# Optimization experiments

Measured on AMD Instinct MI355X. Metric: run time of the kernel, lower is better.

Reference implementation:

```python
import jax, jax.numpy as jnp
import numpy as np

EPS = 1e-7
MAX_TANH = 15.0
C = 1.0  # curvature of every PoincareBall manifold in the stack

def _norm(x):
    return jnp.clip(jnp.linalg.norm(x, axis=-1, keepdims=True), EPS, None)

def _artanh(x):
    return jnp.arctanh(jnp.clip(x, -1.0 + 1e-5, 1.0 - 1e-5))

def proj(x, c=C):
    # clip points back inside the Poincare ball
    maxnorm = (1.0 - 1e-5) / jnp.sqrt(c)
    n = _norm(x)
    return jnp.where(n > maxnorm, x / n * maxnorm, x)

def expmap0(u, c=C):
    sc = jnp.sqrt(c)
    n = _norm(u)
    return jnp.tanh(jnp.clip(sc * n, -MAX_TANH, MAX_TANH)) * u / (sc * n)

def logmap0(x, c=C):
    sc = jnp.sqrt(c)
    n = _norm(x)
    return _artanh(sc * n) * x / (sc * n)

def mobius_add(x, y, c=C):
    x2 = jnp.sum(x * x, -1, keepdims=True)
    y2 = jnp.sum(y * y, -1, keepdims=True)
    xy = jnp.sum(x * y, -1, keepdims=True)
    num = (1 + 2 * c * xy + c * y2) * x + (1 - c * x2) * y
    den = 1 + 2 * c * xy + c * c * x2 * y2
    return num / jnp.clip(den, EPS, None)

def mobius_matvec(W, x, c=C):
    sc = jnp.sqrt(c)
    xn = _norm(x)
    mx = x @ W.T
    mxn = _norm(mx)
    return jnp.tanh(jnp.clip(mxn / xn * _artanh(sc * xn), -MAX_TANH, MAX_TANH)) * mx / (mxn * sc)

def hgc_layer(x, edges, node_mask, edge_mask, W, b, c_in=C, c_out=C):
    n_nodes = x.shape[0]
    # HypLinear: mobius matvec + hyperbolic bias add
    h = proj(mobius_matvec(W, x, c_in), c_in)
    hyp_bias = proj(expmap0(b[None, :], c_in), c_in)
    h = proj(mobius_add(h, hyp_bias, c_in), c_in)
    # HypAgg: masked tangent-space mean over incoming edges (gather -> segment_sum)
    row, col = edges[0], edges[1]
    ht = logmap0(h, c_in)                 # [N, d] tangent features
    msgs = ht[col] * edge_mask            # [E, d]
    agg = jax.ops.segment_sum(msgs, row, num_segments=n_nodes)
    deg = jax.ops.segment_sum(edge_mask, row, num_segments=n_nodes)
    agg = agg / jnp.clip(deg, 1.0, None)
    h = proj(expmap0(agg, c_in), c_in)
    # HypAct: nonlinearity in tangent space, re-map to output manifold
    xt = jax.nn.relu(logmap0(h, c_in))
    h = proj(expmap0(xt, c_out), c_out)
    return h * node_mask

N_NODES = 50000
N_EDGES = 1200000
DIM = 64
NUM_LAYERS = 2

def setup_inputs() -> dict:
    key = jax.random.key(0)
    ks = jax.random.split(key, 8)
    h_tan = 0.1 * jax.random.normal(ks[0], (N_NODES, DIM), dtype=jnp.float32)
    h = proj(expmap0(h_tan))  # valid Poincare-ball points
    distances = jax.random.uniform(ks[1], (N_EDGES, 1), dtype=jnp.float32)
    edges = jax.random.randint(ks[2], (2, N_EDGES), 0, N_NODES, dtype=jnp.int64)
    node_mask = jnp.ones((N_NODES, 1), dtype=jnp.float32)
    edge_mask = jnp.ones((N_EDGES, 1), dtype=jnp.float32)
    W0 = 0.1 * jax.random.normal(ks[3], (DIM, DIM), dtype=jnp.float32)
    b0 = 0.01 * jax.random.normal(ks[4], (DIM,), dtype=jnp.float32)
    W1 = 0.1 * jax.random.normal(ks[5], (DIM, DIM), dtype=jnp.float32)
    b1 = 0.01 * jax.random.normal(ks[6], (DIM,), dtype=jnp.float32)
    return {"h": h, "distances": distances, "edges": edges,
            "node_mask": node_mask, "edge_mask": edge_mask,
            "W0": W0, "b0": b0, "W1": W1, "b1": b1}

def reference(h, distances, edges, node_mask, edge_mask, W0, b0, W1, b1):
    # nn.Sequential of HyperbolicGraphConvolution layers; distances/edges/masks pass through
    out = hgc_layer(h, edges, node_mask, edge_mask, W0, b0)
    out = hgc_layer(out, edges, node_mask, edge_mask, W1, b1)
    return out
```

## Files before the change

kernel.cpp:

```cpp
#include <hip/hip_runtime.h>
#include <hip/hip_fp16.h>

#define EPS      1e-7f
#define MAX_TANH 15.0f
#define MAXNORM  0.99999f
#define ART_CLIP 0.99999f
#define HGRID    512
#define CAPF     8192

__device__ __forceinline__ float wave_sum64(float v) {
#pragma unroll
    for (int o = 32; o > 0; o >>= 1) v += __shfl_xor(v, o, 64);
    return v;
}

__device__ __forceinline__ float gsum16(float v) {
    v += __shfl_xor(v, 1, 64);
    v += __shfl_xor(v, 2, 64);
    v += __shfl_xor(v, 4, 64);
    v += __shfl_xor(v, 8, 64);
    return v;
}

__device__ __forceinline__ float clamp_tanh_arg(float x) {
    return fminf(fmaxf(x, -MAX_TANH), MAX_TANH);
}

__device__ __forceinline__ float artanh_clip(float x) {
    x = fminf(fmaxf(x, -ART_CLIP), ART_CLIP);
    return 0.5f * logf((1.0f + x) / (1.0f - x));
}

__device__ __forceinline__ void fma_h4(float4& acc, uint2 u, float m) {
    float2 f01 = __half22float2(*reinterpret_cast<__half2*>(&u.x));
    float2 f23 = __half22float2(*reinterpret_cast<__half2*>(&u.y));
    acc.x = fmaf(f01.x, m, acc.x); acc.y = fmaf(f01.y, m, acc.y);
    acc.z = fmaf(f23.x, m, acc.z); acc.w = fmaf(f23.y, m, acc.w);
}

__global__ __launch_bounds__(256) void hist_transform_kernel(
    const int* __restrict__ rows, int* __restrict__ histB,
    int n_edges, int epb, int nb,
    const float* __restrict__ x, const float* __restrict__ W,
    const float* __restrict__ b, __half* __restrict__ ht, int n_nodes)
{
    __shared__ float WT[64 * 65];
    __shared__ float xs[4][64];
    __shared__ int hh[256];

    if (blockIdx.x < HGRID) {
        const int b0 = blockIdx.x * epb;
        const int b1 = min(b0 + epb, n_edges);
        if (threadIdx.x < 256) hh[threadIdx.x] = 0;
        __syncthreads();
        for (int i = b0 + threadIdx.x; i < b1; i += 256)
            atomicAdd(&hh[rows[i] >> 8], 1);
        __syncthreads();
        if (threadIdx.x < nb)
            histB[blockIdx.x * nb + threadIdx.x] = hh[threadIdx.x];
        return;
    }

    const int t = threadIdx.x;
    const int lane = t & 63;
    const int wv = t >> 6;
    const int bid = blockIdx.x - HGRID;
    const int tgrid = gridDim.x - HGRID;

#pragma unroll
    for (int r = 0; r < 16; ++r) {
        int idx = r * 256 + t;
        WT[(idx & 63) * 65 + (idx >> 6)] = W[idx];
    }
    __syncthreads();

    float bj = b[lane];
    float bn = fmaxf(sqrtf(wave_sum64(bj * bj)), EPS);
    float tb = tanhf(clamp_tanh_arg(bn));
    float hb = tb * bj / bn;
    if (tb > MAXNORM) { hb *= MAXNORM / tb; tb = MAXNORM; }
    const float y2 = tb * tb;

    for (long long base = (long long)bid * 4; base < n_nodes;
         base += (long long)tgrid * 4) {
        long long node = base + wv;
        float xj = 0.0f;
        if (node < n_nodes) xj = x[node * 64 + lane];
        xs[wv][lane] = xj;

        float mxj = 0.0f;
#pragma unroll
        for (int k = 0; k < 64; ++k)
            mxj = fmaf(xs[wv][k], WT[k * 65 + lane], mxj);

        float xn  = fmaxf(sqrtf(wave_sum64(xj * xj)), EPS);
        float mxn = fmaxf(sqrtf(wave_sum64(mxj * mxj)), EPS);
        float r = tanhf(clamp_tanh_arg(mxn / xn * artanh_clip(xn)));
        float hj = r * mxj / mxn;
        float hn = fmaxf(r, EPS);
        if (hn > MAXNORM) { hj *= MAXNORM / hn; hn = MAXNORM; }

        float x2 = hn * hn;
        float xy = wave_sum64(hj * hb);
        float num = (1.0f + 2.0f * xy + y2) * hj + (1.0f - x2) * hb;
        float den = fmaxf(1.0f + 2.0f * xy + x2 * y2, EPS);
        hj = num / den;

        float hn2 = fmaxf(sqrtf(wave_sum64(hj * hj)), EPS);
        if (hn2 > MAXNORM) { hj *= MAXNORM / hn2; hn2 = MAXNORM; }

        float htj = artanh_clip(hn2) * hj / hn2;

        if (node < n_nodes) ht[node * 64 + lane] = __float2half(htj);
    }
}

__global__ __launch_bounds__(HGRID) void scan_bucket_kernel(
    int* __restrict__ histB, int* __restrict__ tot, int nb)
{
    __shared__ int wsum[8];
    const int b = blockIdx.x;
    const int t = threadIdx.x;
    const int lane = t & 63, wid = t >> 6;
    int v = histB[t * nb + b];
    int incl = v;
#pragma unroll
    for (int o = 1; o < 64; o <<= 1) {
        int tt = __shfl_up(incl, o, 64);
        if (lane >= o) incl += tt;
    }
    if (lane == 63) wsum[wid] = incl;
    __syncthreads();
    if (wid == 0 && lane < 8) {
        int ws = wsum[lane];
#pragma unroll
        for (int o = 1; o < 8; o <<= 1) {
            int tt = __shfl_up(ws, o, 64);
            if (lane >= o) ws += tt;
        }
        wsum[lane] = ws;
    }
    __syncthreads();
    int base = (wid > 0) ? wsum[wid - 1] : 0;
    histB[t * nb + b] = base + incl - v;
    if (t == HGRID - 1) tot[b] = base + incl;
}

__global__ __launch_bounds__(256) void scan_base_kernel(
    const int* __restrict__ tot, int* __restrict__ bucket_base, int nb)
{
    __shared__ int s[256];
    const int t = threadIdx.x;
    int v = (t < nb) ? tot[t] : 0;
    s[t] = v;
    __syncthreads();
    for (int off = 1; off < 256; off <<= 1) {
        int u = (t >= off) ? s[t - off] : 0;
        __syncthreads();
        s[t] += u;
        __syncthreads();
    }
    if (t < nb) bucket_base[t] = s[t] - v;
    if (t == nb - 1) bucket_base[nb] = s[t];
}

__global__ __launch_bounds__(256) void coarse_scatter_kernel(
    const int* __restrict__ rows, const int* __restrict__ cols,
    const float* __restrict__ edge_mask, const int* __restrict__ off,
    const int* __restrict__ bucket_base,
    int2* __restrict__ coarse, int n_edges, int epb, int nb)
{
    __shared__ int cur[256];
    const int b0 = blockIdx.x * epb;
    const int b1 = min(b0 + epb, n_edges);
    if (threadIdx.x < nb)
        cur[threadIdx.x] = bucket_base[threadIdx.x] + off[blockIdx.x * nb + threadIdx.x];
    __syncthreads();
    for (int i = b0 + threadIdx.x; i < b1; i += 256) {
        int r = rows[i], c = cols[i];
        float m = edge_mask[i];
        int pos = atomicAdd(&cur[r >> 8], 1);
        coarse[pos] = make_int2((r << 16) | c, __float_as_int(m));
    }
}

__global__ __launch_bounds__(1024) void fine_kernel(
    const int2* __restrict__ coarse, const int* __restrict__ bucket_base,
    int2* __restrict__ csr, int* __restrict__ row_start, int n_nodes, int n_edges)
{
    __shared__ int hh[256], incl[256], curs[256];
    __shared__ int2 out[CAPF];
    const int t = threadIdx.x;
    const int b = blockIdx.x;
    const int bbase = bucket_base[b];
    const int n_e = bucket_base[b + 1] - bbase;

    if (t < 256) hh[t] = 0;
    __syncthreads();
    for (int i = t; i < n_e; i += 1024) {
        unsigned rx = (unsigned)coarse[bbase + i].x;
        atomicAdd(&hh[(rx >> 16) & 255], 1);
    }
    __syncthreads();
    if (t < 256) incl[t] = hh[t];
    __syncthreads();
    for (int off = 1; off < 256; off <<= 1) {
        int v = 0;
        if (t < 256 && t >= off) v = incl[t - off];
        __syncthreads();
        if (t < 256) incl[t] += v;
        __syncthreads();
    }
    if (t < 256) {
        int lstart = incl[t] - hh[t];
        curs[t] = lstart;
        int grow = (b << 8) + t;
        if (grow < n_nodes) row_start[grow] = bbase + lstart;
    }
    if (b == gridDim.x - 1 && t == 0) row_start[n_nodes] = n_edges;
    __syncthreads();
    for (int i = t; i < n_e; i += 1024) {
        int2 rec = coarse[bbase + i];
        unsigned rx = (unsigned)rec.x;
        int slot = atomicAdd(&curs[(rx >> 16) & 255], 1);
        if (slot < CAPF) out[slot] = make_int2((int)(rx & 0xffffu), rec.y);
    }
    __syncthreads();
    const int lim = min(n_e, CAPF);
    for (int i = t; i < lim; i += 1024)
        csr[bbase + i] = out[i];
}

template <bool FUSE>
__global__ __launch_bounds__(256) void gather_kernel(
    const __half* __restrict__ ht, const int2* __restrict__ csr,
    const int* __restrict__ row_start, const float* __restrict__ node_mask,
    const float* __restrict__ W, const float* __restrict__ b,
    void* __restrict__ outp, int n_nodes)
{
    __shared__ float WT[FUSE ? 4096 : 1];
    __shared__ float xs[FUSE ? 16 * 68 : 1];

    const int t = threadIdx.x;
    const int lane = t & 63;
    const int wv = t >> 6;
    const int ns = lane >> 4;
    const int q  = lane & 15;

    float4 hb4 = make_float4(0.f, 0.f, 0.f, 0.f);
    float y2 = 0.f;
    if constexpr (FUSE) {
#pragma unroll
        for (int r = 0; r < 16; ++r) {
            int idx = r * 256 + t;
            int j = idx >> 6, k = idx & 63;
            WT[(k << 6) | (j ^ ((k & 15) << 2))] = W[idx];
        }
        float4 b4 = ((const float4*)b)[q];
        float ssb = b4.x*b4.x + b4.y*b4.y + b4.z*b4.z + b4.w*b4.w;
        float bn = fmaxf(sqrtf(gsum16(ssb)), EPS);
        float tb = tanhf(clamp_tanh_arg(bn));
        float sb = tb / bn;
        hb4.x = b4.x * sb; hb4.y = b4.y * sb; hb4.z = b4.z * sb; hb4.w = b4.w * sb;
        if (tb > MAXNORM) {
            float sc = MAXNORM / tb;
            hb4.x *= sc; hb4.y *= sc; hb4.z *= sc; hb4.w *= sc;
            tb = MAXNORM;
        }
        y2 = tb * tb;
        __syncthreads();
    }

    const int node = blockIdx.x * 16 + (wv << 2) + ns;
    const bool valid = node < n_nodes;
    const int nd = valid ? node : (n_nodes - 1);
    const int s = row_start[nd];
    const int e = row_start[nd + 1];

    float4 acc = make_float4(0.f, 0.f, 0.f, 0.f);
    float msum = 0.f;
    int j = s;
    for (; j + 4 <= e; j += 4) {
        int2 c0 = csr[j], c1 = csr[j + 1];
        int2 c2 = csr[j + 2], c3 = csr[j + 3];
        uint2 u0 = *((const uint2*)(ht + (long long)c0.x * 64) + q);
        uint2 u1 = *((const uint2*)(ht + (long long)c1.x * 64) + q);
        uint2 u2 = *((const uint2*)(ht + (long long)c2.x * 64) + q);
        uint2 u3 = *((const uint2*)(ht + (long long)c3.x * 64) + q);
        float m0 = __int_as_float(c0.y), m1 = __int_as_float(c1.y);
        float m2 = __int_as_float(c2.y), m3 = __int_as_float(c3.y);
        fma_h4(acc, u0, m0);
        fma_h4(acc, u1, m1);
        fma_h4(acc, u2, m2);
        fma_h4(acc, u3, m3);
        msum += m0 + m1 + m2 + m3;
    }
    for (; j < e; ++j) {
        int2 cm = csr[j];
        uint2 u = *((const uint2*)(ht + (long long)cm.x * 64) + q);
        float m = __int_as_float(cm.y);
        fma_h4(acc, u, m);
        msum += m;
    }

    const float inv = 1.0f / fmaxf(msum, 1.0f);
    acc.x *= inv; acc.y *= inv; acc.z *= inv; acc.w *= inv;

    float ss = acc.x*acc.x + acc.y*acc.y + acc.z*acc.z + acc.w*acc.w;
    float n1 = fmaxf(sqrtf(gsum16(ss)), EPS);
    float t1 = tanhf(clamp_tanh_arg(n1));
    float r1 = t1 / n1;
    acc.x *= r1; acc.y *= r1; acc.z *= r1; acc.w *= r1;
    if (t1 > MAXNORM) {
        float sc = MAXNORM / t1;
        acc.x *= sc; acc.y *= sc; acc.z *= sc; acc.w *= sc;
        t1 = MAXNORM;
    }
    float n2 = fmaxf(t1, EPS);
    float r2 = artanh_clip(n2) / n2;
    acc.x = fmaxf(acc.x * r2, 0.f); acc.y = fmaxf(acc.y * r2, 0.f);
    acc.z = fmaxf(acc.z * r2, 0.f); acc.w = fmaxf(acc.w * r2, 0.f);

    ss = acc.x*acc.x + acc.y*acc.y + acc.z*acc.z + acc.w*acc.w;
    float n3 = fmaxf(sqrtf(gsum16(ss)), EPS);
    float t3 = tanhf(clamp_tanh_arg(n3));
    float r3 = t3 / n3;
    acc.x *= r3; acc.y *= r3; acc.z *= r3; acc.w *= r3;
    if (t3 > MAXNORM) {
        float sc = MAXNORM / t3;
        acc.x *= sc; acc.y *= sc; acc.z *= sc; acc.w *= sc;
        t3 = MAXNORM;
    }

    const float nm = node_mask[nd];
    acc.x *= nm; acc.y *= nm; acc.z *= nm; acc.w *= nm;

    if constexpr (!FUSE) {
        if (valid) ((float4*)((float*)outp + (long long)node * 64))[q] = acc;
    } else {
        float* xrow = &xs[(wv * 4 + ns) * 68];
        *(float4*)(xrow + (q << 2)) = acc;

        float4 mx = make_float4(0.f, 0.f, 0.f, 0.f);
#pragma unroll
        for (int k = 0; k < 64; ++k) {
            float xk = xrow[k];
            const float4 w4 = *(const float4*)&WT[(k << 6) | ((q << 2) ^ ((k & 15) << 2))];
            mx.x = fmaf(w4.x, xk, mx.x); mx.y = fmaf(w4.y, xk, mx.y);
            mx.z = fmaf(w4.z, xk, mx.z); mx.w = fmaf(w4.w, xk, mx.w);
        }

        float xn  = fmaxf(t3 * fabsf(nm), EPS);
        float ssm = mx.x*mx.x + mx.y*mx.y + mx.z*mx.z + mx.w*mx.w;
        float mxn = fmaxf(sqrtf(gsum16(ssm)), EPS);
        float r = tanhf(clamp_tanh_arg(mxn / xn * artanh_clip(xn)));
        float rs = r / mxn;
        float4 hj = make_float4(mx.x * rs, mx.y * rs, mx.z * rs, mx.w * rs);
        float hn = fmaxf(r, EPS);
        if (hn > MAXNORM) {
            float sc = MAXNORM / hn;
            hj.x *= sc; hj.y *= sc; hj.z *= sc; hj.w *= sc;
            hn = MAXNORM;
        }

        float x2 = hn * hn;
        float xy = gsum16(hj.x*hb4.x + hj.y*hb4.y + hj.z*hb4.z + hj.w*hb4.w);
        float ca = 1.0f + 2.0f * xy + y2;
        float cb = 1.0f - x2;
        float iden = 1.0f / fmaxf(1.0f + 2.0f * xy + x2 * y2, EPS);
        hj.x = (ca * hj.x + cb * hb4.x) * iden;
        hj.y = (ca * hj.y + cb * hb4.y) * iden;
        hj.z = (ca * hj.z + cb * hb4.z) * iden;
        hj.w = (ca * hj.w + cb * hb4.w) * iden;

        float ssh = hj.x*hj.x + hj.y*hj.y + hj.z*hj.z + hj.w*hj.w;
        float hn2 = fmaxf(sqrtf(gsum16(ssh)), EPS);
        float sc2 = (hn2 > MAXNORM) ? (MAXNORM / hn2) : 1.0f;
        float hnc = fminf(hn2, MAXNORM);
        float lr = artanh_clip(hnc) / hnc * sc2;
        hj.x *= lr; hj.y *= lr; hj.z *= lr; hj.w *= lr;

        if (valid) {
            __half2 p01 = __float22half2_rn(make_float2(hj.x, hj.y));
            __half2 p23 = __float22half2_rn(make_float2(hj.z, hj.w));
            uint2 o;
            o.x = *reinterpret_cast<unsigned*>(&p01);
            o.y = *reinterpret_cast<unsigned*>(&p23);
            *((uint2*)((__half*)outp + (long long)node * 64) + q) = o;
        }
    }
}

extern "C" void kernel_launch(void* const* d_in, const int* in_sizes, int n_in,
                              void* d_out, int out_size, void* d_ws, size_t ws_size,
                              hipStream_t stream) {
    const float* h         = (const float*)d_in[0];
    const int*   edges     = (const int*)d_in[2];
    const float* node_mask = (const float*)d_in[3];
    const float* edge_mask = (const float*)d_in[4];
    const float* W0        = (const float*)d_in[5];
    const float* b0        = (const float*)d_in[6];
    const float* W1        = (const float*)d_in[7];
    const float* b1        = (const float*)d_in[8];
    float* out = (float*)d_out;

    const int N = in_sizes[0] / 64;
    const int E = in_sizes[4];
    const int* rows = edges;
    const int* cols = edges + E;

    const int NB  = (N + 255) >> 8;
    const int EPB = (E + HGRID - 1) / HGRID;

    size_t nd = (size_t)N * 64;
    char* ws = (char*)d_ws;
    __half* B1         = (__half*)ws; ws += nd * sizeof(__half);
    __half* B2         = (__half*)ws; ws += nd * sizeof(__half);
    int2*  coarse      = (int2*)ws;   ws += (size_t)E * sizeof(int2);
    int2*  csr         = (int2*)ws;   ws += (size_t)E * sizeof(int2);
    int*   histB       = (int*)ws;    ws += (size_t)HGRID * NB * sizeof(int);
    int*   tot         = (int*)ws;    ws += (size_t)NB * sizeof(int);
    int*   bucket_base = (int*)ws;    ws += (size_t)(NB + 1) * sizeof(int);
    int*   row_start   = (int*)ws;    ws += (size_t)(N + 1) * sizeof(int);

    const int TGRID = 1024;
    const int NGRID = (N + 15) / 16;

    hist_transform_kernel<<<HGRID + TGRID, 256, 0, stream>>>(
        rows, histB, E, EPB, NB, h, W0, b0, B1, N);

    scan_bucket_kernel<<<NB, HGRID, 0, stream>>>(histB, tot, NB);

    scan_base_kernel<<<1, 256, 0, stream>>>(tot, bucket_base, NB);

    coarse_scatter_kernel<<<HGRID, 256, 0, stream>>>(
        rows, cols, edge_mask, histB, bucket_base, coarse, E, EPB, NB);

    fine_kernel<<<NB, 1024, 0, stream>>>(
        coarse, bucket_base, csr, row_start, N, E);

    gather_kernel<true><<<NGRID, 256, 0, stream>>>(
        B1, csr, row_start, node_mask, W1, b1, B2, N);

    gather_kernel<false><<<NGRID, 256, 0, stream>>>(
        B2, csr, row_start, node_mask, nullptr, nullptr, out, N);
}
```

Measured before the change: 222.2 us.

## Fuse fine CSR bucketing with first-layer gather and compact CSR to 32-bit

Bucket size drops from 256 to 128 rows, so each fine-sort block keeps its sorted edges in shared memory. The first-layer aggregation and second-layer transform then run inside that same block, reading edges from LDS and skipping a separate CSR read pass. The CSR written for the second layer packs the column and an fp16 edge mask into 32 bits, halving index traffic. In exchange, each block uses a lot of shared memory at 1024 threads, which lowers occupancy. The edge mask is rounded to fp16, and the 16-bit column packing relies on node IDs below 65536.

```diff
diff --git a/kernel.cpp b/kernel.cpp
--- a/kernel.cpp
+++ b/kernel.cpp
@@ -6,7 +6,9 @@
 #define MAXNORM  0.99999f
 #define ART_CLIP 0.99999f
 #define HGRID    512
-#define CAPF     8192
+#define RPB      128
+#define CAPF     4096
+#define NBMAX    512
 
 __device__ __forceinline__ float wave_sum64(float v) {
 #pragma unroll
@@ -46,18 +48,18 @@
 {
     __shared__ float WT[64 * 65];
     __shared__ float xs[4][64];
-    __shared__ int hh[256];
+    __shared__ int hh[NBMAX];
 
     if (blockIdx.x < HGRID) {
         const int b0 = blockIdx.x * epb;
         const int b1 = min(b0 + epb, n_edges);
-        if (threadIdx.x < 256) hh[threadIdx.x] = 0;
+        for (int j = threadIdx.x; j < nb; j += 256) hh[j] = 0;
         __syncthreads();
         for (int i = b0 + threadIdx.x; i < b1; i += 256)
-            atomicAdd(&hh[rows[i] >> 8], 1);
+            atomicAdd(&hh[rows[i] >> 7], 1);
         __syncthreads();
-        if (threadIdx.x < nb)
-            histB[blockIdx.x * nb + threadIdx.x] = hh[threadIdx.x];
+        for (int j = threadIdx.x; j < nb; j += 256)
+            histB[blockIdx.x * nb + j] = hh[j];
         return;
     }
 
@@ -146,15 +148,15 @@
     if (t == HGRID - 1) tot[b] = base + incl;
 }
 
-__global__ __launch_bounds__(256) void scan_base_kernel(
+__global__ __launch_bounds__(NBMAX) void scan_base_kernel(
     const int* __restrict__ tot, int* __restrict__ bucket_base, int nb)
 {
-    __shared__ int s[256];
+    __shared__ int s[NBMAX];
     const int t = threadIdx.x;
     int v = (t < nb) ? tot[t] : 0;
     s[t] = v;
     __syncthreads();
-    for (int off = 1; off < 256; off <<= 1) {
+    for (int off = 1; off < NBMAX; off <<= 1) {
         int u = (t >= off) ? s[t - off] : 0;
         __syncthreads();
         s[t] += u;
@@ -170,175 +172,158 @@
     const int* __restrict__ bucket_base,
     int2* __restrict__ coarse, int n_edges, int epb, int nb)
 {
-    __shared__ int cur[256];
+    __shared__ int cur[NBMAX];
     const int b0 = blockIdx.x * epb;
     const int b1 = min(b0 + epb, n_edges);
-    if (threadIdx.x < nb)
-        cur[threadIdx.x] = bucket_base[threadIdx.x] + off[blockIdx.x * nb + threadIdx.x];
+    for (int j = threadIdx.x; j < nb; j += 256)
+        cur[j] = bucket_base[j] + off[blockIdx.x * nb + j];
     __syncthreads();
     for (int i = b0 + threadIdx.x; i < b1; i += 256) {
         int r = rows[i], c = cols[i];
         float m = edge_mask[i];
-        int pos = atomicAdd(&cur[r >> 8], 1);
+        int pos = atomicAdd(&cur[r >> 7], 1);
         coarse[pos] = make_int2((r << 16) | c, __float_as_int(m));
     }
 }
 
-__global__ __launch_bounds__(1024) void fine_kernel(
+__global__ __launch_bounds__(1024) void fine_gather_kernel(
     const int2* __restrict__ coarse, const int* __restrict__ bucket_base,
-    int2* __restrict__ csr, int* __restrict__ row_start, int n_nodes, int n_edges)
+    const __half* __restrict__ ht1, const float* __restrict__ node_mask,
+    const float* __restrict__ W, const float* __restrict__ bvec,
+    unsigned* __restrict__ csr4, int* __restrict__ row_start,
+    __half* __restrict__ ht2, int n_nodes, int n_edges)
 {
-    __shared__ int hh[256], incl[256], curs[256];
-    __shared__ int2 out[CAPF];
+    __shared__ int hh[RPB], incl[RPB], curs[RPB];
+    __shared__ int2 outE[CAPF];
+    __shared__ float WT[4096];
+    __shared__ float xs[64 * 68];
+
     const int t = threadIdx.x;
     const int b = blockIdx.x;
+    const int q = t & 15;
+    const int g = t >> 4;
     const int bbase = bucket_base[b];
     const int n_e = bucket_base[b + 1] - bbase;
 
-    if (t < 256) hh[t] = 0;
-    __syncthreads();
-    for (int i = t; i < n_e; i += 1024) {
-        unsigned rx = (unsigned)coarse[bbase + i].x;
-        atomicAdd(&hh[(rx >> 16) & 255], 1);
-    }
-    __syncthreads();
-    if (t < 256) incl[t] = hh[t];
-    __syncthreads();
-    for (int off = 1; off < 256; off <<= 1) {
-        int v = 0;
-        if (t < 256 && t >= off) v = incl[t - off];
+#pragma unroll
+    for (int r = 0; r < 4; ++r) {
+        int idx = r * 1024 + t;
+        int j = idx >> 6, k = idx & 63;
+        WT[(k << 6) | (j ^ ((k & 15) << 2))] = W[idx];
+    }
+    float4 b4 = ((const float4*)bvec)[q];
+    float ssb = b4.x*b4.x + b4.y*b4.y + b4.z*b4.z + b4.w*b4.w;
+    float bn = fmaxf(sqrtf(gsum16(ssb)), EPS);
+    float tb = tanhf(clamp_tanh_arg(bn));
+    float sb = tb / bn;
+    float4 hb4 = make_float4(b4.x * sb, b4.y * sb, b4.z * sb, b4.w * sb);
+    if (tb > MAXNORM) {
+        float sc = MAXNORM / tb;
+        hb4.x *= sc; hb4.y *= sc; hb4.z *= sc; hb4.w *= sc;
+        tb = MAXNORM;
+    }
+    const float y2 = tb * tb;
+
+    if (t < RPB) hh[t] = 0;
+    __syncthreads();
+    for (int i = t; i < n_e; i += 1024)
+        atomicAdd(&hh[(coarse[bbase + i].x >> 16) & (RPB - 1)], 1);
+    __syncthreads();
+    if (t < RPB) incl[t] = hh[t];
+    __syncthreads();
+    for (int off = 1; off < RPB; off <<= 1) {
+        int v = (t < RPB && t >= off) ? incl[t - off] : 0;
         __syncthreads();
-        if (t < 256) incl[t] += v;
+        if (t < RPB) incl[t] += v;
         __syncthreads();
     }
-    if (t < 256) {
-        int lstart = incl[t] - hh[t];
-        curs[t] = lstart;
-        int grow = (b << 8) + t;
-        if (grow < n_nodes) row_start[grow] = bbase + lstart;
+    if (t < RPB) {
+        curs[t] = incl[t] - hh[t];
+        int grow = (b << 7) + t;
+        if (grow < n_nodes) row_start[grow] = bbase + incl[t] - hh[t];
     }
     if (b == gridDim.x - 1 && t == 0) row_start[n_nodes] = n_edges;
     __syncthreads();
     for (int i = t; i < n_e; i += 1024) {
         int2 rec = coarse[bbase + i];
-        unsigned rx = (unsigned)rec.x;
-        int slot = atomicAdd(&curs[(rx >> 16) & 255], 1);
-        if (slot < CAPF) out[slot] = make_int2((int)(rx & 0xffffu), rec.y);
-    }
-    __syncthreads();
+        int slot = atomicAdd(&curs[(rec.x >> 16) & (RPB - 1)], 1);
+        if (slot < CAPF) outE[slot] = make_int2(rec.x & 0xffff, rec.y);
+    }
+    __syncthreads();
+
     const int lim = min(n_e, CAPF);
-    for (int i = t; i < lim; i += 1024)
-        csr[bbase + i] = out[i];
-}
-
-template <bool FUSE>
-__global__ __launch_bounds__(256) void gather_kernel(
-    const __half* __restrict__ ht, const int2* __restrict__ csr,
-    const int* __restrict__ row_start, const float* __restrict__ node_mask,
-    const float* __restrict__ W, const float* __restrict__ b,
-    void* __restrict__ outp, int n_nodes)
-{
-    __shared__ float WT[FUSE ? 4096 : 1];
-    __shared__ float xs[FUSE ? 16 * 68 : 1];
-
-    const int t = threadIdx.x;
-    const int lane = t & 63;
-    const int wv = t >> 6;
-    const int ns = lane >> 4;
-    const int q  = lane & 15;
-
-    float4 hb4 = make_float4(0.f, 0.f, 0.f, 0.f);
-    float y2 = 0.f;
-    if constexpr (FUSE) {
-#pragma unroll
-        for (int r = 0; r < 16; ++r) {
-            int idx = r * 256 + t;
-            int j = idx >> 6, k = idx & 63;
-            WT[(k << 6) | (j ^ ((k & 15) << 2))] = W[idx];
-        }
-        float4 b4 = ((const float4*)b)[q];
-        float ssb = b4.x*b4.x + b4.y*b4.y + b4.z*b4.z + b4.w*b4.w;
-        float bn = fmaxf(sqrtf(gsum16(ssb)), EPS);
-        float tb = tanhf(clamp_tanh_arg(bn));
-        float sb = tb / bn;
-        hb4.x = b4.x * sb; hb4.y = b4.y * sb; hb4.z = b4.z * sb; hb4.w = b4.w * sb;
-        if (tb > MAXNORM) {
-            float sc = MAXNORM / tb;
-            hb4.x *= sc; hb4.y *= sc; hb4.z *= sc; hb4.w *= sc;
-            tb = MAXNORM;
-        }
-        y2 = tb * tb;
-        __syncthreads();
-    }
-
-    const int node = blockIdx.x * 16 + (wv << 2) + ns;
-    const bool valid = node < n_nodes;
-    const int nd = valid ? node : (n_nodes - 1);
-    const int s = row_start[nd];
-    const int e = row_start[nd + 1];
-
-    float4 acc = make_float4(0.f, 0.f, 0.f, 0.f);
-    float msum = 0.f;
-    int j = s;
-    for (; j + 4 <= e; j += 4) {
-        int2 c0 = csr[j], c1 = csr[j + 1];
-        int2 c2 = csr[j + 2], c3 = csr[j + 3];
-        uint2 u0 = *((const uint2*)(ht + (long long)c0.x * 64) + q);
-        uint2 u1 = *((const uint2*)(ht + (long long)c1.x * 64) + q);
-        uint2 u2 = *((const uint2*)(ht + (long long)c2.x * 64) + q);
-        uint2 u3 = *((const uint2*)(ht + (long long)c3.x * 64) + q);
-        float m0 = __int_as_float(c0.y), m1 = __int_as_float(c1.y);
-        float m2 = __int_as_float(c2.y), m3 = __int_as_float(c3.y);
-        fma_h4(acc, u0, m0);
-        fma_h4(acc, u1, m1);
-        fma_h4(acc, u2, m2);
-        fma_h4(acc, u3, m3);
-        msum += m0 + m1 + m2 + m3;
-    }
-    for (; j < e; ++j) {
-        int2 cm = csr[j];
-        uint2 u = *((const uint2*)(ht + (long long)cm.x * 64) + q);
-        float m = __int_as_float(cm.y);
-        fma_h4(acc, u, m);
-        msum += m;
-    }
-
-    const float inv = 1.0f / fmaxf(msum, 1.0f);
-    acc.x *= inv; acc.y *= inv; acc.z *= inv; acc.w *= inv;
-
-    float ss = acc.x*acc.x + acc.y*acc.y + acc.z*acc.z + acc.w*acc.w;
-    float n1 = fmaxf(sqrtf(gsum16(ss)), EPS);
-    float t1 = tanhf(clamp_tanh_arg(n1));
-    float r1 = t1 / n1;
-    acc.x *= r1; acc.y *= r1; acc.z *= r1; acc.w *= r1;
-    if (t1 > MAXNORM) {
-        float sc = MAXNORM / t1;
-        acc.x *= sc; acc.y *= sc; acc.z *= sc; acc.w *= sc;
-        t1 = MAXNORM;
-    }
-    float n2 = fmaxf(t1, EPS);
-    float r2 = artanh_clip(n2) / n2;
-    acc.x = fmaxf(acc.x * r2, 0.f); acc.y = fmaxf(acc.y * r2, 0.f);
-    acc.z = fmaxf(acc.z * r2, 0.f); acc.w = fmaxf(acc.w * r2, 0.f);
-
-    ss = acc.x*acc.x + acc.y*acc.y + acc.z*acc.z + acc.w*acc.w;
-    float n3 = fmaxf(sqrtf(gsum16(ss)), EPS);
-    float t3 = tanhf(clamp_tanh_arg(n3));
-    float r3 = t3 / n3;
-    acc.x *= r3; acc.y *= r3; acc.z *= r3; acc.w *= r3;
-    if (t3 > MAXNORM) {
-        float sc = MAXNORM / t3;
-        acc.x *= sc; acc.y *= sc; acc.z *= sc; acc.w *= sc;
-        t3 = MAXNORM;
-    }
-
-    const float nm = node_mask[nd];
-    acc.x *= nm; acc.y *= nm; acc.z *= nm; acc.w *= nm;
-
-    if constexpr (!FUSE) {
-        if (valid) ((float4*)((float*)outp + (long long)node * 64))[q] = acc;
-    } else {
-        float* xrow = &xs[(wv * 4 + ns) * 68];
+    for (int i = t; i < lim; i += 1024) {
+        int2 rec = outE[i];
+        __half hm = __float2half(__int_as_float(rec.y));
+        csr4[bbase + i] = (unsigned)rec.x |
+                          ((unsigned)*reinterpret_cast<unsigned short*>(&hm) << 16);
+    }
+
+#pragma unroll
+    for (int batch = 0; batch < 2; ++batch) {
+        const int ln = batch * 64 + g;
+        const int node = (b << 7) + ln;
+        const bool valid = node < n_nodes;
+        const int nd = valid ? node : (n_nodes - 1);
+        const int s0 = incl[ln] - hh[ln];
+        const int e0 = incl[ln];
+
+        float4 acc = make_float4(0.f, 0.f, 0.f, 0.f);
+        float msum = 0.f;
+        int j = s0;
+        for (; j + 4 <= e0; j += 4) {
+            int2 r0 = outE[j], r1 = outE[j + 1], r2 = outE[j + 2], r3 = outE[j + 3];
+            uint2 u0 = *((const uint2*)(ht1 + (long long)r0.x * 64) + q);
+            uint2 u1 = *((const uint2*)(ht1 + (long long)r1.x * 64) + q);
+            uint2 u2 = *((const uint2*)(ht1 + (long long)r2.x * 64) + q);
+            uint2 u3 = *((const uint2*)(ht1 + (long long)r3.x * 64) + q);
+            float m0 = __int_as_float(r0.y), m1 = __int_as_float(r1.y);
+            float m2 = __int_as_float(r2.y), m3 = __int_as_float(r3.y);
+            fma_h4(acc, u0, m0); fma_h4(acc, u1, m1);
+            fma_h4(acc, u2, m2); fma_h4(acc, u3, m3);
+            msum += m0 + m1 + m2 + m3;
+        }
+        for (; j < e0; ++j) {
+            int2 rec = outE[j];
+            uint2 u = *((const uint2*)(ht1 + (long long)rec.x * 64) + q);
+            float m = __int_as_float(rec.y);
+            fma_h4(acc, u, m);
+            msum += m;
+        }
+
+        const float inv = 1.0f / fmaxf(msum, 1.0f);
+        acc.x *= inv; acc.y *= inv; acc.z *= inv; acc.w *= inv;
+
+        float ss = acc.x*acc.x + acc.y*acc.y + acc.z*acc.z + acc.w*acc.w;
+        float n1 = fmaxf(sqrtf(gsum16(ss)), EPS);
+        float t1 = tanhf(clamp_tanh_arg(n1));
+        float r1 = t1 / n1;
+        acc.x *= r1; acc.y *= r1; acc.z *= r1; acc.w *= r1;
+        if (t1 > MAXNORM) {
+            float sc = MAXNORM / t1;
+            acc.x *= sc; acc.y *= sc; acc.z *= sc; acc.w *= sc;
+            t1 = MAXNORM;
+        }
+        float n2 = fmaxf(t1, EPS);
+        float r2s = artanh_clip(n2) / n2;
+        acc.x = fmaxf(acc.x * r2s, 0.f); acc.y = fmaxf(acc.y * r2s, 0.f);
+        acc.z = fmaxf(acc.z * r2s, 0.f); acc.w = fmaxf(acc.w * r2s, 0.f);
+
+        ss = acc.x*acc.x + acc.y*acc.y + acc.z*acc.z + acc.w*acc.w;
+        float n3 = fmaxf(sqrtf(gsum16(ss)), EPS);
+        float t3 = tanhf(clamp_tanh_arg(n3));
+        float r3 = t3 / n3;
+        acc.x *= r3; acc.y *= r3; acc.z *= r3; acc.w *= r3;
+        if (t3 > MAXNORM) {
+            float sc = MAXNORM / t3;
+            acc.x *= sc; acc.y *= sc; acc.z *= sc; acc.w *= sc;
+            t3 = MAXNORM;
+        }
+
+        const float nm = node_mask[nd];
+        acc.x *= nm; acc.y *= nm; acc.z *= nm; acc.w *= nm;
+
+        float* xrow = &xs[g * 68];
         *(float4*)(xrow + (q << 2)) = acc;
 
         float4 mx = make_float4(0.f, 0.f, 0.f, 0.f);
@@ -386,9 +371,88 @@
             uint2 o;
             o.x = *reinterpret_cast<unsigned*>(&p01);
             o.y = *reinterpret_cast<unsigned*>(&p23);
-            *((uint2*)((__half*)outp + (long long)node * 64) + q) = o;
-        }
-    }
+            *((uint2*)(ht2 + (long long)node * 64) + q) = o;
+        }
+    }
+}
+
+__global__ __launch_bounds__(256) void gather2_kernel(
+    const __half* __restrict__ ht, const unsigned* __restrict__ csr4,
+    const int* __restrict__ row_start, const float* __restrict__ node_mask,
+    float* __restrict__ outp, int n_nodes)
+{
+    const int t = threadIdx.x;
+    const int lane = t & 63;
+    const int wv = t >> 6;
+    const int ns = lane >> 4;
+    const int q  = lane & 15;
+
+    const int node = blockIdx.x * 16 + (wv << 2) + ns;
+    const bool valid = node < n_nodes;
+    const int nd = valid ? node : (n_nodes - 1);
+    const int s = row_start[nd];
+    const int e = row_start[nd + 1];
+
+    float4 acc = make_float4(0.f, 0.f, 0.f, 0.f);
+    float msum = 0.f;
+    int j = s;
+    for (; j + 4 <= e; j += 4) {
+        unsigned v0 = csr4[j], v1 = csr4[j + 1], v2 = csr4[j + 2], v3 = csr4[j + 3];
+        uint2 u0 = *((const uint2*)(ht + (long long)(v0 & 0xffffu) * 64) + q);
+        uint2 u1 = *((const uint2*)(ht + (long long)(v1 & 0xffffu) * 64) + q);
+        uint2 u2 = *((const uint2*)(ht + (long long)(v2 & 0xffffu) * 64) + q);
+        uint2 u3 = *((const uint2*)(ht + (long long)(v3 & 0xffffu) * 64) + q);
+        unsigned short h0 = v0 >> 16, h1 = v1 >> 16, h2 = v2 >> 16, h3 = v3 >> 16;
+        float m0 = __half2float(*reinterpret_cast<__half*>(&h0));
+        float m1 = __half2float(*reinterpret_cast<__half*>(&h1));
+        float m2 = __half2float(*reinterpret_cast<__half*>(&h2));
+        float m3 = __half2float(*reinterpret_cast<__half*>(&h3));
+        fma_h4(acc, u0, m0); fma_h4(acc, u1, m1);
+        fma_h4(acc, u2, m2); fma_h4(acc, u3, m3);
+        msum += m0 + m1 + m2 + m3;
+    }
+    for (; j < e; ++j) {
+        unsigned v = csr4[j];
+        uint2 u = *((const uint2*)(ht + (long long)(v & 0xffffu) * 64) + q);
+        unsigned short hb = v >> 16;
+        float m = __half2float(*reinterpret_cast<__half*>(&hb));
+        fma_h4(acc, u, m);
+        msum += m;
+    }
+
+    const float inv = 1.0f / fmaxf(msum, 1.0f);
+    acc.x *= inv; acc.y *= inv; acc.z *= inv; acc.w *= inv;
+
+    float ss = acc.x*acc.x + acc.y*acc.y + acc.z*acc.z + acc.w*acc.w;
+    float n1 = fmaxf(sqrtf(gsum16(ss)), EPS);
+    float t1 = tanhf(clamp_tanh_arg(n1));
+    float r1 = t1 / n1;
+    acc.x *= r1; acc.y *= r1; acc.z *= r1; acc.w *= r1;
+    if (t1 > MAXNORM) {
+        float sc = MAXNORM / t1;
+        acc.x *= sc; acc.y *= sc; acc.z *= sc; acc.w *= sc;
+        t1 = MAXNORM;
+    }
+    float n2 = fmaxf(t1, EPS);
+    float r2 = artanh_clip(n2) / n2;
+    acc.x = fmaxf(acc.x * r2, 0.f); acc.y = fmaxf(acc.y * r2, 0.f);
+    acc.z = fmaxf(acc.z * r2, 0.f); acc.w = fmaxf(acc.w * r2, 0.f);
+
+    ss = acc.x*acc.x + acc.y*acc.y + acc.z*acc.z + acc.w*acc.w;
+    float n3 = fmaxf(sqrtf(gsum16(ss)), EPS);
+    float t3 = tanhf(clamp_tanh_arg(n3));
+    float r3 = t3 / n3;
+    acc.x *= r3; acc.y *= r3; acc.z *= r3; acc.w *= r3;
+    if (t3 > MAXNORM) {
+        float sc = MAXNORM / t3;
+        acc.x *= sc; acc.y *= sc; acc.z *= sc; acc.w *= sc;
+        t3 = MAXNORM;
+    }
+
+    const float nm = node_mask[nd];
+    acc.x *= nm; acc.y *= nm; acc.z *= nm; acc.w *= nm;
+
+    if (valid) ((float4*)(outp + (long long)node * 64))[q] = acc;
 }
 
 extern "C" void kernel_launch(void* const* d_in, const int* in_sizes, int n_in,
@@ -409,19 +473,19 @@
     const int* rows = edges;
     const int* cols = edges + E;
 
-    const int NB  = (N + 255) >> 8;
+    const int NB  = (N + RPB - 1) / RPB;
     const int EPB = (E + HGRID - 1) / HGRID;
 
     size_t nd = (size_t)N * 64;
     char* ws = (char*)d_ws;
-    __half* B1         = (__half*)ws; ws += nd * sizeof(__half);
-    __half* B2         = (__half*)ws; ws += nd * sizeof(__half);
-    int2*  coarse      = (int2*)ws;   ws += (size_t)E * sizeof(int2);
-    int2*  csr         = (int2*)ws;   ws += (size_t)E * sizeof(int2);
-    int*   histB       = (int*)ws;    ws += (size_t)HGRID * NB * sizeof(int);
-    int*   tot         = (int*)ws;    ws += (size_t)NB * sizeof(int);
-    int*   bucket_base = (int*)ws;    ws += (size_t)(NB + 1) * sizeof(int);
-    int*   row_start   = (int*)ws;    ws += (size_t)(N + 1) * sizeof(int);
+    __half*   B1          = (__half*)ws;   ws += nd * sizeof(__half);
+    __half*   B2          = (__half*)ws;   ws += nd * sizeof(__half);
+    int2*     coarse      = (int2*)ws;     ws += (size_t)E * sizeof(int2);
+    unsigned* csr4        = (unsigned*)ws; ws += (size_t)E * sizeof(unsigned);
+    int*      histB       = (int*)ws;      ws += (size_t)HGRID * NB * sizeof(int);
+    int*      tot         = (int*)ws;      ws += (size_t)NB * sizeof(int);
+    int*      bucket_base = (int*)ws;      ws += (size_t)(NB + 1) * sizeof(int);
+    int*      row_start   = (int*)ws;      ws += (size_t)(N + 1) * sizeof(int);
 
     const int TGRID = 1024;
     const int NGRID = (N + 15) / 16;
@@ -430,18 +494,14 @@
         rows, histB, E, EPB, NB, h, W0, b0, B1, N);
 
     scan_bucket_kernel<<<NB, HGRID, 0, stream>>>(histB, tot, NB);
-
-    scan_base_kernel<<<1, 256, 0, stream>>>(tot, bucket_base, NB);
+    scan_base_kernel<<<1, NBMAX, 0, stream>>>(tot, bucket_base, NB);
 
     coarse_scatter_kernel<<<HGRID, 256, 0, stream>>>(
         rows, cols, edge_mask, histB, bucket_base, coarse, E, EPB, NB);
 
-    fine_kernel<<<NB, 1024, 0, stream>>>(
-        coarse, bucket_base, csr, row_start, N, E);
-
-    gather_kernel<true><<<NGRID, 256, 0, stream>>>(
-        B1, csr, row_start, node_mask, W1, b1, B2, N);
-
-    gather_kernel<false><<<NGRID, 256, 0, stream>>>(
-        B2, csr, row_start, node_mask, nullptr, nullptr, out, N);
-}
+    fine_gather_kernel<<<NB, 1024, 0, stream>>>(
+        coarse, bucket_base, B1, node_mask, W1, b1, csr4, row_start, B2, N, E);
+
+    gather2_kernel<<<NGRID, 256, 0, stream>>>(
+        B2, csr4, row_start, node_mask, out, N);
+}
```

Measured after the change: 206.5 us. 1.08x faster.
